# Optimization experiments

Measured on AMD Instinct MI355X. Metric: run time of the kernel, lower is better.

The kernel has to match this reference:

```python
import jax, jax.numpy as jnp
import numpy as np

N_NODES = 50000
N_EDGES = 600000
C = 128
T = 2          # layer index t
NU = 1         # DRew nu parameter
EPS = 0.0      # GIN eps


def mlp(x, W1, b1, W2, b2):
    # instantiate_mlp with final_activation=False, batch_norm=False:
    # Linear -> ReLU -> Linear
    return jax.nn.relu(x @ W1 + b1) @ W2 + b2


def setup_inputs() -> dict:
    key = jax.random.key(0)
    ks = jax.random.split(key, 16)
    node_embeddings = jax.random.normal(ks[0], (T + 1, N_NODES, C), dtype=jnp.float32)
    edge_index = jax.random.randint(ks[1], (2, N_EDGES), 0, N_NODES, dtype=jnp.int32)
    edge_weights = jax.random.randint(ks[2], (N_EDGES,), 1, T + 2, dtype=jnp.int32)  # hops 1..3
    s = 1.0 / np.sqrt(C)
    def lin(k):
        kw, kb = jax.random.split(k)
        return (jax.random.uniform(kw, (C, C), jnp.float32, -s, s),
                jax.random.uniform(kb, (C,), jnp.float32, -s, s))
    loop_W1, loop_b1 = lin(ks[3]); loop_W2, loop_b2 = lin(ks[4])
    rel_W1, rel_b1 = lin(ks[5]); rel_W2, rel_b2 = lin(ks[6])
    # T higher-hop MLPs (k = 2 .. T+1), stacked along axis 0
    hh1 = [lin(k) for k in jax.random.split(ks[7], T)]
    hh2 = [lin(k) for k in jax.random.split(ks[8], T)]
    hh_W1 = jnp.stack([w for w, _ in hh1]); hh_b1 = jnp.stack([b for _, b in hh1])
    hh_W2 = jnp.stack([w for w, _ in hh2]); hh_b2 = jnp.stack([b for _, b in hh2])
    hop_coef = jax.random.normal(ks[9], (T + 1,), dtype=jnp.float32)
    return dict(t=T, node_embeddings=node_embeddings, edge_index=edge_index,
                edge_weights=edge_weights,
                loop_W1=loop_W1, loop_b1=loop_b1, loop_W2=loop_W2, loop_b2=loop_b2,
                rel_W1=rel_W1, rel_b1=rel_b1, rel_W2=rel_W2, rel_b2=rel_b2,
                hh_W1=hh_W1, hh_b1=hh_b1, hh_W2=hh_W2, hh_b2=hh_b2,
                hop_coef=hop_coef)


def reference(t, node_embeddings, edge_index, edge_weights,
              loop_W1, loop_b1, loop_W2, loop_b2,
              rel_W1, rel_b1, rel_W2, rel_b2,
              hh_W1, hh_b1, hh_W2, hh_b2, hop_coef):
    x_t = node_embeddings[t]                       # [N, C]
    n = x_t.shape[0]
    row, col = edge_index[0], edge_index[1]        # sparse A: out[row] += X[col]
    dt = x_t.dtype

    hops = []
    # hop 1: relational MLP on current-layer embeddings
    h1 = mlp(x_t, rel_W1, rel_b1, rel_W2, rel_b2)
    m1 = (edge_weights == 1).astype(dt)[:, None]
    hops.append(jax.ops.segment_sum(h1[col] * m1, row, num_segments=n))
    # hops k = 2 .. t+1: per-hop MLP on delayed embeddings (DRew)
    for k in range(2, t + 2):
        delay = max(0, k - NU)
        hk = mlp(node_embeddings[t - delay],
                 hh_W1[k - 2], hh_b1[k - 2], hh_W2[k - 2], hh_b2[k - 2])
        mk = (edge_weights == k).astype(dt)[:, None]
        hops.append(jax.ops.segment_sum(hk[col] * mk, row, num_segments=n))

    by_hop = jnp.stack(hops)                       # [t+1, N, C]
    self_term = mlp((1.0 + EPS) * x_t, loop_W1, loop_b1, loop_W2, loop_b2)
    return self_term + jnp.einsum('k,knc->nc', hop_coef, by_hop)
```

## Files before the change

kernel.cpp:

```cpp
#include <hip/hip_runtime.h>

#define N_NODES 50000
#define N_EDGES 600000
#define C 128
#define STRIPS 3125
#define N_TASKS 4
#define MLP_BLOCKS 256
#define MAXOVF 16384

typedef __bf16 bf16;
typedef __attribute__((ext_vector_type(8))) __bf16 bf16x8;
typedef __attribute__((ext_vector_type(4))) __bf16 bf16x4;
typedef __attribute__((ext_vector_type(2))) __bf16 bf16x2;
typedef __attribute__((ext_vector_type(4))) float f32x4;
typedef __attribute__((ext_vector_type(2))) float f32x2;

struct PtrsV { const void* p[8]; };

__device__ __forceinline__ int bf16_wild(unsigned short w) {
    int exp = (w >> 7) & 0xFF;
    int mant = w & 0x7F;
    if (exp == 0xFF) return 1;
    if (exp >= 133) return 1;
    if (exp == 0) return mant != 0 ? 1 : 0;
    if (exp <= 114) return 1;
    return 0;
}

__global__ void __launch_bounds__(256) detect_zero_kernel(
    const unsigned short* __restrict__ emb,
    const unsigned short* __restrict__ w,
    const unsigned short* __restrict__ b,
    const unsigned short* __restrict__ hc,
    int* __restrict__ flags,
    int* __restrict__ z0, int* __restrict__ z1,
    int* __restrict__ ovf_cnt)
{
    if (blockIdx.x == 0) {
        int lane = threadIdx.x;
        if (lane >= 64) return;
        int ce = 0, cw = 0, cb = 0, ch = 0;
        for (int j = 0; j < 4; ++j) {
            ce += bf16_wild(emb[lane * 4 + j]);
            cw += bf16_wild(w[lane * 4 + j]);
        }
        for (int j = 0; j < 2; ++j) cb += bf16_wild(b[lane * 2 + j]);
        if (lane < 3) ch = bf16_wild(hc[lane]);
        for (int off = 32; off > 0; off >>= 1) {
            ce += __shfl_down(ce, off);
            cw += __shfl_down(cw, off);
            cb += __shfl_down(cb, off);
            ch += __shfl_down(ch, off);
        }
        if (lane == 0) {
            int wf = (cw >= 16) ? 1 : 0;
            flags[0] = (ce >= 16) ? 1 : 0;
            flags[1] = wf;
            flags[2] = (cb >= 8) ? 1 : 0;
            flags[3] = (ch > 0) ? 1 : wf;
        }
    } else {
        int i = (blockIdx.x - 1) * 256 + threadIdx.x;
        if (i < N_NODES) { z0[i] = 0; z1[i] = 0; }
        if (blockIdx.x == 1 && threadIdx.x == 0) *ovf_cnt = 0;
    }
}

__global__ void __launch_bounds__(256) pack_kernel(
    PtrsV wmats, PtrsV bvecs, const void* hc_raw,
    const int* __restrict__ flags,
    bf16* __restrict__ pw, float* __restrict__ cbias, float* __restrict__ ccoef)
{
    int tid = blockIdx.x * 256 + threadIdx.x;
    int wf = flags[1], bfl = flags[2], hf = flags[3];
    if (tid < 8 * 16384) {
        int m    = tid >> 14;
        int r    = tid & 16383;
        int j    = r & 7;
        int lane = (r >> 3) & 63;
        int n0   = (r >> 9) & 7;
        int kk   = r >> 12;
        int k = kk * 32 + (lane >> 4) * 8 + j;
        int n = n0 * 16 + (lane & 15);
        int idx = k * C + n + ((m == 4 || m == 5) ? 16384 : 0);
        float v = wf ? ((const float*)wmats.p[m])[idx]
                     : (float)((const bf16*)wmats.p[m])[idx];
        pw[tid] = (bf16)v;
    } else if (tid < 8 * 16384 + 1024) {
        int j = tid - 8 * 16384;
        int m = j >> 7, n = j & 127;
        int idx = n + ((m == 4 || m == 5) ? 128 : 0);
        float v = bfl ? ((const float*)bvecs.p[m])[idx]
                      : (float)((const bf16*)bvecs.p[m])[idx];
        cbias[j] = v;
    } else if (tid < 8 * 16384 + 1024 + 3) {
        int i = tid - (8 * 16384 + 1024);
        float v = hf ? ((const float*)hc_raw)[i]
                     : (float)((const bf16*)hc_raw)[i];
        ccoef[i] = v;
    }
}

__global__ __launch_bounds__(512, 2) void mlp_kernel(
    const void* __restrict__ emb_raw,
    const bf16* __restrict__ pw,
    const float* __restrict__ cbias,
    const float* __restrict__ ccoef,
    const int* __restrict__ flags,
    bf16* __restrict__ h,
    bf16* __restrict__ hs)
{
    __shared__ bf16 sW[32768];
    __shared__ bf16 sH[8][16][136];
    const int tid  = threadIdx.x;
    const int wave = tid >> 6, lane = tid & 63;
    const int task  = blockIdx.x & 3;
    const int bslot = blockIdx.x >> 2;
    const int lrow = lane & 15, lquad = lane >> 4;
    bf16 (*sh)[136] = sH[wave];

    const int m1_of[4] = {0, 2, 4, 6};
    const int ly_of[4] = {2, 1, 0, 2};
    const int m1 = m1_of[task];
    const float oscale = (task == 0) ? ccoef[0] : (task == 1) ? ccoef[1]
                       : (task == 2) ? ccoef[2] : 1.0f;
    bf16* outp = (task == 3) ? hs : (h + (size_t)task * N_NODES * C);
    const int emb_f32 = flags[0];
    const size_t lbase = (size_t)ly_of[task] * N_NODES * C;

    {
        const f32x4* src = (const f32x4*)(pw + (size_t)m1 * 16384);
        f32x4* dst = (f32x4*)sW;
        #pragma unroll
        for (int i = 0; i < 8; ++i)
            dst[i * 512 + tid] = src[i * 512 + tid];
    }
    __syncthreads();
    const bf16x8* w1v = (const bf16x8*)sW;
    const bf16x8* w2v = w1v + 2048;

    float b1f[8], b2f[8];
    #pragma unroll
    for (int n0 = 0; n0 < 8; ++n0) {
        b1f[n0] = cbias[m1 * 128 + n0 * 16 + lrow];
        b2f[n0] = cbias[(m1 + 1) * 128 + n0 * 16 + lrow];
    }

    int s = bslot * 8 + wave;
    f32x4 u[8]; bf16x8 araw[4];

    {
        size_t xb = lbase + (size_t)(s * 16 + lrow) * C + lquad * 8;
        if (emb_f32) {
            const float* xf = (const float*)emb_raw + xb;
            #pragma unroll
            for (int kk = 0; kk < 4; ++kk) {
                u[kk * 2]     = *(const f32x4*)(xf + kk * 32);
                u[kk * 2 + 1] = *(const f32x4*)(xf + kk * 32 + 4);
            }
        } else {
            const bf16* x16 = (const bf16*)emb_raw + xb;
            #pragma unroll
            for (int kk = 0; kk < 4; ++kk)
                araw[kk] = *(const bf16x8*)(x16 + kk * 32);
        }
    }

    while (s < STRIPS) {
        const int snext = s + 512;

        bf16x8 af[4];
        if (emb_f32) {
            #pragma unroll
            for (int kk = 0; kk < 4; ++kk) {
                f32x4 u0 = u[kk * 2], u1 = u[kk * 2 + 1];
                bf16x8 v;
                v[0]=(bf16)u0[0]; v[1]=(bf16)u0[1]; v[2]=(bf16)u0[2]; v[3]=(bf16)u0[3];
                v[4]=(bf16)u1[0]; v[5]=(bf16)u1[1]; v[6]=(bf16)u1[2]; v[7]=(bf16)u1[3];
                af[kk] = v;
            }
        } else {
            #pragma unroll
            for (int kk = 0; kk < 4; ++kk) af[kk] = araw[kk];
        }

        if (snext < STRIPS) {
            size_t xb = lbase + (size_t)(snext * 16 + lrow) * C + lquad * 8;
            if (emb_f32) {
                const float* xf = (const float*)emb_raw + xb;
                #pragma unroll
                for (int kk = 0; kk < 4; ++kk) {
                    u[kk * 2]     = *(const f32x4*)(xf + kk * 32);
                    u[kk * 2 + 1] = *(const f32x4*)(xf + kk * 32 + 4);
                }
            } else {
                const bf16* x16 = (const bf16*)emb_raw + xb;
                #pragma unroll
                for (int kk = 0; kk < 4; ++kk)
                    araw[kk] = *(const bf16x8*)(x16 + kk * 32);
            }
        }

        #pragma unroll
        for (int n0 = 0; n0 < 8; ++n0) {
            bf16x8 bv0 = w1v[0 * 512 + n0 * 64 + lane];
            bf16x8 bv1 = w1v[1 * 512 + n0 * 64 + lane];
            bf16x8 bv2 = w1v[2 * 512 + n0 * 64 + lane];
            bf16x8 bv3 = w1v[3 * 512 + n0 * 64 + lane];
            int n = n0 * 16 + lrow;
            float bias = b1f[n0];
            f32x4 a4 = {0.f, 0.f, 0.f, 0.f};
            a4 = __builtin_amdgcn_mfma_f32_16x16x32_bf16(af[0], bv0, a4, 0, 0, 0);
            a4 = __builtin_amdgcn_mfma_f32_16x16x32_bf16(af[1], bv1, a4, 0, 0, 0);
            a4 = __builtin_amdgcn_mfma_f32_16x16x32_bf16(af[2], bv2, a4, 0, 0, 0);
            a4 = __builtin_amdgcn_mfma_f32_16x16x32_bf16(af[3], bv3, a4, 0, 0, 0);
            #pragma unroll
            for (int r = 0; r < 4; ++r) {
                float v = a4[r] + bias;
                v = v > 0.f ? v : 0.f;
                sh[lquad * 4 + r][n] = (bf16)v;
            }
        }

        bf16x8 ah[4];
        #pragma unroll
        for (int kk = 0; kk < 4; ++kk)
            ah[kk] = *(const bf16x8*)(&sh[lrow][kk * 32 + lquad * 8]);

        #pragma unroll
        for (int n0 = 0; n0 < 8; ++n0) {
            bf16x8 bv0 = w2v[0 * 512 + n0 * 64 + lane];
            bf16x8 bv1 = w2v[1 * 512 + n0 * 64 + lane];
            bf16x8 bv2 = w2v[2 * 512 + n0 * 64 + lane];
            bf16x8 bv3 = w2v[3 * 512 + n0 * 64 + lane];
            int n = n0 * 16 + lrow;
            float bias = b2f[n0];
            f32x4 a4 = {0.f, 0.f, 0.f, 0.f};
            a4 = __builtin_amdgcn_mfma_f32_16x16x32_bf16(ah[0], bv0, a4, 0, 0, 0);
            a4 = __builtin_amdgcn_mfma_f32_16x16x32_bf16(ah[1], bv1, a4, 0, 0, 0);
            a4 = __builtin_amdgcn_mfma_f32_16x16x32_bf16(ah[2], bv2, a4, 0, 0, 0);
            a4 = __builtin_amdgcn_mfma_f32_16x16x32_bf16(ah[3], bv3, a4, 0, 0, 0);
            #pragma unroll
            for (int r = 0; r < 4; ++r)
                sh[lquad * 4 + r][n] = (bf16)((a4[r] + bias) * oscale);
        }

        {
            int row = lane >> 2;
            int cs  = (lane & 3) * 32;
            bf16* dst = outp + (size_t)(s * 16) * C;
            #pragma unroll
            for (int j = 0; j < 4; ++j) {
                bf16x8 v = *(const bf16x8*)(&sh[row][cs + j * 8]);
                *(bf16x8*)(dst + (size_t)row * C + cs + j * 8) = v;
            }
        }

        s = snext;
    }
}

__global__ void __launch_bounds__(256) bucket_kernel(
    const int* __restrict__ erow, const int* __restrict__ ecol,
    const int* __restrict__ ew,
    int* __restrict__ cursor, int* __restrict__ edata,
    int* __restrict__ ovf_cnt, int* __restrict__ ovf, int cap)
{
    int e = blockIdx.x * 256 + threadIdx.x;
    if (e >= N_EDGES) return;
    int dst = erow[e];
    int val = (ecol[e] << 2) | (ew[e] - 1);
    int pos = atomicAdd(&cursor[dst], 1);
    if (pos < cap) {
        edata[(size_t)dst * cap + pos] = val;
    } else {
        int o = atomicAdd(ovf_cnt, 1);
        if (o < MAXOVF) { ovf[2 * o] = dst; ovf[2 * o + 1] = val; }
    }
}

__global__ void __launch_bounds__(256) hist_kernel(
    const int* __restrict__ erow, int* __restrict__ deg)
{
    int e = blockIdx.x * 256 + threadIdx.x;
    if (e >= N_EDGES) return;
    atomicAdd(&deg[erow[e]], 1);
}

__device__ __forceinline__ int wave_incl_scan(int v, int lane) {
    int x = v;
    #pragma unroll
    for (int d = 1; d < 64; d <<= 1) {
        int t = __shfl_up(x, d);
        if (lane >= d) x += t;
    }
    return x;
}

__global__ void __launch_bounds__(256) scanA_kernel(
    const int* __restrict__ deg, int* __restrict__ offsets, int* __restrict__ btot)
{
    __shared__ int swave[4];
    int b = blockIdx.x, tid = threadIdx.x;
    int i = b * 256 + tid;
    int lane = tid & 63, wv = tid >> 6;
    int v = (i < N_NODES) ? deg[i] : 0;
    int x = wave_incl_scan(v, lane);
    if (lane == 63) swave[wv] = x;
    __syncthreads();
    int w0 = swave[0], w1 = swave[1], w2 = swave[2], w3 = swave[3];
    int wp = (wv > 0 ? w0 : 0) + (wv > 1 ? w1 : 0) + (wv > 2 ? w2 : 0);
    if (i < N_NODES) offsets[i] = wp + x - v;
    if (tid == 0) btot[b] = w0 + w1 + w2 + w3;
}

__global__ void __launch_bounds__(256) scanB_kernel(
    const int* __restrict__ btot, int* __restrict__ bbase, int nblk)
{
    __shared__ int swave[4];
    int tid = threadIdx.x;
    int lane = tid & 63, wv = tid >> 6;
    int v = (tid < nblk) ? btot[tid] : 0;
    int x = wave_incl_scan(v, lane);
    if (lane == 63) swave[wv] = x;
    __syncthreads();
    int w0 = swave[0], w1 = swave[1], w2 = swave[2], w3 = swave[3];
    int wp = (wv > 0 ? w0 : 0) + (wv > 1 ? w1 : 0) + (wv > 2 ? w2 : 0);
    if (tid < nblk) bbase[tid] = wp + x - v;
}

__global__ void __launch_bounds__(256) scanC_kernel(
    const int* __restrict__ bbase, int* __restrict__ offsets, int* __restrict__ cursor)
{
    int i = blockIdx.x * 256 + threadIdx.x;
    if (i < N_NODES) {
        int o = offsets[i] + bbase[blockIdx.x];
        offsets[i] = o;
        cursor[i] = o;
    }
    if (i == 0) offsets[N_NODES] = N_EDGES;
}

__global__ void __launch_bounds__(256) fill_kernel(
    const int* __restrict__ erow, const int* __restrict__ ecol,
    const int* __restrict__ ew,
    int* __restrict__ cursor, int* __restrict__ edata)
{
    int e = blockIdx.x * 256 + threadIdx.x;
    if (e >= N_EDGES) return;
    int dst = erow[e];
    int pos = atomicAdd(&cursor[dst], 1);
    edata[pos] = (ecol[e] << 2) | (ew[e] - 1);
}

__global__ void __launch_bounds__(256) gather_kernel(
    const int* __restrict__ offsets, const int* __restrict__ cursor,
    const int* __restrict__ edata,
    const bf16* __restrict__ h,
    const bf16* __restrict__ hs,
    void* __restrict__ out,
    const int* __restrict__ flags, int cap)
{
    const int node = blockIdx.x * 4 + (threadIdx.x >> 6);
    if (node >= N_NODES) return;
    const int lane = threadIdx.x & 63;
    const int c = lane * 2;

    bf16x2 sv = *(const bf16x2*)(hs + (size_t)node * C + c);
    float a0 = (float)sv[0], a1 = (float)sv[1];

    int s, e;
    const int* ebase;
    if (cap) {
        int d = cursor[node];
        if (d > cap) d = cap;
        s = 0; e = d;
        ebase = edata + (size_t)node * cap;
    } else {
        s = offsets[node]; e = offsets[node + 1];
        ebase = edata;
    }

    for (int base = s; base < e; base += 64) {
        int idx = base + lane;
        int ed_i = (idx < e) ? ebase[idx] : 0;
        int cnt = e - base; if (cnt > 64) cnt = 64;
        int j = 0;
        for (; j + 8 <= cnt; j += 8) {
            float t0 = 0.f, t1 = 0.f;
            #pragma unroll
            for (int u = 0; u < 8; ++u) {
                int ed = __shfl(ed_i, j + u);
                bf16x2 v = *(const bf16x2*)(h + (size_t)(ed & 3) * (N_NODES * C)
                                              + (size_t)(ed >> 2) * C + c);
                t0 += (float)v[0];
                t1 += (float)v[1];
            }
            a0 += t0; a1 += t1;
        }
        for (; j + 4 <= cnt; j += 4) {
            int e0 = __shfl(ed_i, j);
            int e1 = __shfl(ed_i, j + 1);
            int e2 = __shfl(ed_i, j + 2);
            int e3 = __shfl(ed_i, j + 3);
            bf16x2 v0 = *(const bf16x2*)(h + (size_t)(e0 & 3) * (N_NODES * C) + (size_t)(e0 >> 2) * C + c);
            bf16x2 v1 = *(const bf16x2*)(h + (size_t)(e1 & 3) * (N_NODES * C) + (size_t)(e1 >> 2) * C + c);
            bf16x2 v2 = *(const bf16x2*)(h + (size_t)(e2 & 3) * (N_NODES * C) + (size_t)(e2 >> 2) * C + c);
            bf16x2 v3 = *(const bf16x2*)(h + (size_t)(e3 & 3) * (N_NODES * C) + (size_t)(e3 >> 2) * C + c);
            a0 += (float)v0[0] + (float)v1[0] + (float)v2[0] + (float)v3[0];
            a1 += (float)v0[1] + (float)v1[1] + (float)v2[1] + (float)v3[1];
        }
        for (; j < cnt; ++j) {
            int ed = __shfl(ed_i, j);
            bf16x2 v = *(const bf16x2*)(h + (size_t)(ed & 3) * (N_NODES * C) + (size_t)(ed >> 2) * C + c);
            a0 += (float)v[0];
            a1 += (float)v[1];
        }
    }

    if (flags[0]) {
        f32x2 o; o[0] = a0; o[1] = a1;
        *(f32x2*)((float*)out + (size_t)node * C + c) = o;
    } else {
        bf16x2 o; o[0] = (bf16)a0; o[1] = (bf16)a1;
        *(bf16x2*)((bf16*)out + (size_t)node * C + c) = o;
    }
}

__device__ __forceinline__ float bf2f(unsigned short s) {
    unsigned int u = (unsigned int)s << 16;
    float f; __builtin_memcpy(&f, &u, 4); return f;
}
__device__ __forceinline__ unsigned short f2bf(float f) {
    bf16 b = (bf16)f;
    unsigned short s; __builtin_memcpy(&s, &b, 2); return s;
}

__global__ void __launch_bounds__(256) ovf_kernel(
    const int* __restrict__ ovf_cnt, const int* __restrict__ ovf,
    const bf16* __restrict__ h, void* __restrict__ out,
    const int* __restrict__ flags)
{
    int n = *ovf_cnt; if (n > MAXOVF) n = MAXOVF;
    if (n <= 0) return;
    const int gw = (blockIdx.x * 256 + threadIdx.x) >> 6;
    const int lane = threadIdx.x & 63;
    const int nw = gridDim.x * 4;
    const int c = lane * 2;
    for (int i = gw; i < n; i += nw) {
        int dst = ovf[2 * i], val = ovf[2 * i + 1];
        bf16x2 v = *(const bf16x2*)(h + (size_t)(val & 3) * (N_NODES * C)
                                      + (size_t)(val >> 2) * C + c);
        float v0 = (float)v[0], v1 = (float)v[1];
        if (flags[0]) {
            atomicAdd((float*)out + (size_t)dst * C + c, v0);
            atomicAdd((float*)out + (size_t)dst * C + c + 1, v1);
        } else {
            unsigned int* p = (unsigned int*)((bf16*)out + (size_t)dst * C + c);
            unsigned int old = *p, assumed;
            do {
                assumed = old;
                unsigned short lo = assumed & 0xFFFF, hi = assumed >> 16;
                unsigned int nb = (unsigned int)f2bf(bf2f(lo) + v0)
                                | ((unsigned int)f2bf(bf2f(hi) + v1) << 16);
                old = atomicCAS(p, assumed, nb);
            } while (old != assumed);
        }
    }
}

extern "C" void kernel_launch(void* const* d_in, const int* in_sizes, int n_in,
                              void* d_out, int out_size, void* d_ws, size_t ws_size,
                              hipStream_t stream) {
    const void* emb = d_in[1];
    const int*  ei  = (const int*)d_in[2];
    const int*  ew  = (const int*)d_in[3];

    char* base = (char*)d_ws;
    bf16*  h      = (bf16*)base;
    bf16*  hs     = (bf16*)(base + 38400000);
    bf16*  pw     = (bf16*)(base + 51200000);
    float* cbias  = (float*)(base + 51462144);
    float* ccoef  = (float*)(base + 51466240);
    int*   flags  = (int*)(base + 51466256);
    int*   ovf_cnt= (int*)(base + 51466288);
    int*   cursor = (int*)(base + 51466752);

    int*   ovf    = (int*)(base + 51666752);
    int*   bedata = (int*)(base + 51797824);
    size_t avail  = ws_size > 51797824 ? ws_size - 51797824 : 0;
    int cap = (int)(avail / (4ull * N_NODES));
    if (cap > 96) cap = 96;
    cap &= ~15;

    int*   deg    = (int*)(base + 51666752);
    int*   offsets= (int*)(base + 51866752);
    int*   btot   = (int*)(base + 52066816);
    int*   bbase  = (int*)(base + 52067840);
    int*   cedata = (int*)(base + 52068864);

    PtrsV wptr;
    wptr.p[0] = d_in[8];   wptr.p[1] = d_in[10];
    wptr.p[2] = d_in[12];  wptr.p[3] = d_in[14];
    wptr.p[4] = d_in[12];  wptr.p[5] = d_in[14];
    wptr.p[6] = d_in[4];   wptr.p[7] = d_in[6];
    PtrsV bptr;
    bptr.p[0] = d_in[9];   bptr.p[1] = d_in[11];
    bptr.p[2] = d_in[13];  bptr.p[3] = d_in[15];
    bptr.p[4] = d_in[13];  bptr.p[5] = d_in[15];
    bptr.p[6] = d_in[5];   bptr.p[7] = d_in[7];

    const int NBLK = (N_NODES + 255) / 256;
    const int EBLK = (N_EDGES + 255) / 256;
    const int* erow = ei;
    const int* ecol = ei + N_EDGES;

    if (cap >= 32) {
        detect_zero_kernel<<<1 + NBLK, 256, 0, stream>>>(
            (const unsigned short*)emb, (const unsigned short*)d_in[8],
            (const unsigned short*)d_in[9], (const unsigned short*)d_in[16],
            flags, cursor, cursor, ovf_cnt);

        pack_kernel<<<517, 256, 0, stream>>>(wptr, bptr, d_in[16], flags, pw, cbias, ccoef);

        bucket_kernel<<<EBLK, 256, 0, stream>>>(erow, ecol, ew, cursor, bedata,
                                                ovf_cnt, ovf, cap);

        mlp_kernel<<<MLP_BLOCKS, 512, 0, stream>>>(emb, pw, cbias, ccoef, flags, h, hs);

        gather_kernel<<<(N_NODES + 3) / 4, 256, 0, stream>>>(
            cursor, cursor, bedata, h, hs, d_out, flags, cap);

        ovf_kernel<<<32, 256, 0, stream>>>(ovf_cnt, ovf, h, d_out, flags);
    } else {
        detect_zero_kernel<<<1 + NBLK, 256, 0, stream>>>(
            (const unsigned short*)emb, (const unsigned short*)d_in[8],
            (const unsigned short*)d_in[9], (const unsigned short*)d_in[16],
            flags, deg, deg, ovf_cnt);

        pack_kernel<<<517, 256, 0, stream>>>(wptr, bptr, d_in[16], flags, pw, cbias, ccoef);

        hist_kernel<<<EBLK, 256, 0, stream>>>(erow, deg);
        scanA_kernel<<<NBLK, 256, 0, stream>>>(deg, offsets, btot);
        scanB_kernel<<<1, 256, 0, stream>>>(btot, bbase, NBLK);
        scanC_kernel<<<NBLK, 256, 0, stream>>>(bbase, offsets, cursor);
        fill_kernel<<<EBLK, 256, 0, stream>>>(erow, ecol, ew, cursor, cedata);

        mlp_kernel<<<MLP_BLOCKS, 512, 0, stream>>>(emb, pw, cbias, ccoef, flags, h, hs);

        gather_kernel<<<(N_NODES + 3) / 4, 256, 0, stream>>>(
            offsets, cursor, cedata, h, hs, d_out, flags, 0);
    }
}
```

Baseline: 244.9 us.

## Fuse edge bucketing into MLP kernel and widen MLP blocks to 768 threads

The separate bucket kernel is removed, and its edge-bucketing work now runs in extra blocks appended to the MLP kernel's grid. The aim is to overlap the atomic-heavy scatter with the MFMA-bound MLP and save one launch. MLP blocks grow from 512 to 768 threads (12 waves), with the per-wave strip stride and shared staging resized to match. The larger shared-memory footprint (about 116KB per block) may cut how many blocks fit per CU, and bucket blocks now reserve the same large shared allocation as MLP blocks.

```diff
diff --git a/kernel.cpp b/kernel.cpp
--- a/kernel.cpp
+++ b/kernel.cpp
@@ -6,6 +6,8 @@
 #define STRIPS 3125
 #define N_TASKS 4
 #define MLP_BLOCKS 256
+#define MLP_THREADS 768
+#define BUCKET_BLOCKS 782
 #define MAXOVF 16384
 
 typedef __bf16 bf16;
@@ -101,21 +103,43 @@
     }
 }
 
-__global__ __launch_bounds__(512, 2) void mlp_kernel(
+__global__ __launch_bounds__(MLP_THREADS, 3) void mlp_kernel(
     const void* __restrict__ emb_raw,
     const bf16* __restrict__ pw,
     const float* __restrict__ cbias,
     const float* __restrict__ ccoef,
     const int* __restrict__ flags,
     bf16* __restrict__ h,
-    bf16* __restrict__ hs)
+    bf16* __restrict__ hs,
+    const int* __restrict__ erow, const int* __restrict__ ecol,
+    const int* __restrict__ ew,
+    int* __restrict__ cursor, int* __restrict__ bedata,
+    int* __restrict__ ovf_cnt, int* __restrict__ ovf, int cap)
 {
     __shared__ bf16 sW[32768];
-    __shared__ bf16 sH[8][16][136];
+    __shared__ bf16 sH[12][16][136];
     const int tid  = threadIdx.x;
+
+    if (blockIdx.x >= MLP_BLOCKS) {
+        int e = (blockIdx.x - MLP_BLOCKS) * MLP_THREADS + tid;
+        if (e < N_EDGES && cap > 0) {
+            int dst = erow[e];
+            int val = (ecol[e] << 2) | (ew[e] - 1);
+            int pos = atomicAdd(&cursor[dst], 1);
+            if (pos < cap) {
+                bedata[(size_t)dst * cap + pos] = val;
+            } else {
+                int o = atomicAdd(ovf_cnt, 1);
+                if (o < MAXOVF) { ovf[2 * o] = dst; ovf[2 * o + 1] = val; }
+            }
+        }
+        return;
+    }
+
     const int wave = tid >> 6, lane = tid & 63;
     const int task  = blockIdx.x & 3;
     const int bslot = blockIdx.x >> 2;
+    const int widx  = bslot * 12 + wave;
     const int lrow = lane & 15, lquad = lane >> 4;
     bf16 (*sh)[136] = sH[wave];
 
@@ -131,9 +155,8 @@
     {
         const f32x4* src = (const f32x4*)(pw + (size_t)m1 * 16384);
         f32x4* dst = (f32x4*)sW;
-        #pragma unroll
-        for (int i = 0; i < 8; ++i)
-            dst[i * 512 + tid] = src[i * 512 + tid];
+        for (int i = tid; i < 4096; i += MLP_THREADS)
+            dst[i] = src[i];
     }
     __syncthreads();
     const bf16x8* w1v = (const bf16x8*)sW;
@@ -146,7 +169,7 @@
         b2f[n0] = cbias[(m1 + 1) * 128 + n0 * 16 + lrow];
     }
 
-    int s = bslot * 8 + wave;
+    int s = widx;
     f32x4 u[8]; bf16x8 araw[4];
 
     {
@@ -167,7 +190,7 @@
     }
 
     while (s < STRIPS) {
-        const int snext = s + 512;
+        const int snext = s + 768;
 
         bf16x8 af[4];
         if (emb_f32) {
@@ -257,25 +280,6 @@
         }
 
         s = snext;
-    }
-}
-
-__global__ void __launch_bounds__(256) bucket_kernel(
-    const int* __restrict__ erow, const int* __restrict__ ecol,
-    const int* __restrict__ ew,
-    int* __restrict__ cursor, int* __restrict__ edata,
-    int* __restrict__ ovf_cnt, int* __restrict__ ovf, int cap)
-{
-    int e = blockIdx.x * 256 + threadIdx.x;
-    if (e >= N_EDGES) return;
-    int dst = erow[e];
-    int val = (ecol[e] << 2) | (ew[e] - 1);
-    int pos = atomicAdd(&cursor[dst], 1);
-    if (pos < cap) {
-        edata[(size_t)dst * cap + pos] = val;
-    } else {
-        int o = atomicAdd(ovf_cnt, 1);
-        if (o < MAXOVF) { ovf[2 * o] = dst; ovf[2 * o + 1] = val; }
     }
 }
 
@@ -523,10 +527,9 @@
 
         pack_kernel<<<517, 256, 0, stream>>>(wptr, bptr, d_in[16], flags, pw, cbias, ccoef);
 
-        bucket_kernel<<<EBLK, 256, 0, stream>>>(erow, ecol, ew, cursor, bedata,
-                                                ovf_cnt, ovf, cap);
-
-        mlp_kernel<<<MLP_BLOCKS, 512, 0, stream>>>(emb, pw, cbias, ccoef, flags, h, hs);
+        mlp_kernel<<<MLP_BLOCKS + BUCKET_BLOCKS, MLP_THREADS, 0, stream>>>(
+            emb, pw, cbias, ccoef, flags, h, hs,
+            erow, ecol, ew, cursor, bedata, ovf_cnt, ovf, cap);
 
         gather_kernel<<<(N_NODES + 3) / 4, 256, 0, stream>>>(
             cursor, cursor, bedata, h, hs, d_out, flags, cap);
@@ -546,7 +549,9 @@
         scanC_kernel<<<NBLK, 256, 0, stream>>>(bbase, offsets, cursor);
         fill_kernel<<<EBLK, 256, 0, stream>>>(erow, ecol, ew, cursor, cedata);
 
-        mlp_kernel<<<MLP_BLOCKS, 512, 0, stream>>>(emb, pw, cbias, ccoef, flags, h, hs);
+        mlp_kernel<<<MLP_BLOCKS, MLP_THREADS, 0, stream>>>(
+            emb, pw, cbias, ccoef, flags, h, hs,
+            erow, ecol, ew, cursor, cedata, ovf_cnt, ovf, 0);
 
         gather_kernel<<<(N_NODES + 3) / 4, 256, 0, stream>>>(
             offsets, cursor, cedata, h, hs, d_out, flags, 0);
```

New measurement: 288.4 us. +17.7%, slower.
